# Optimization experiments

Measured on AMD Instinct MI355X. Metric: run time of the kernel, lower is better.

Reference implementation:

```python
import jax, jax.numpy as jnp
import numpy as np

N_NODES = 100000
N_EDGES = 6400000
NUM_FEATURES = 128
NUM_CLASSES = 10


def _gcn_norm(edge_index, num_nodes):
    # PyG GCNConv default: add self-loops, symmetric normalization
    src, dst = edge_index[0], edge_index[1]
    loop = jnp.arange(num_nodes, dtype=src.dtype)
    src = jnp.concatenate([src, loop])
    dst = jnp.concatenate([dst, loop])
    deg = jax.ops.segment_sum(jnp.ones_like(dst, dtype=jnp.float32), dst,
                              num_segments=num_nodes)
    dinv = jnp.where(deg > 0, jax.lax.rsqrt(deg), 0.0)
    norm = dinv[src] * dinv[dst]  # [E + N]
    return src, dst, norm


def _gcn_conv(x, W, b, src, dst, norm, num_nodes):
    h = x @ W                              # [N, out] small feature matmul
    msg = h[src] * norm[:, None]           # gather + per-edge scale
    agg = jax.ops.segment_sum(msg, dst, num_segments=num_nodes)  # scatter-add
    return agg + b


def setup_inputs() -> dict:
    key = jax.random.key(0)
    ks = jax.random.split(key, 10)
    x = jax.random.normal(ks[0], (N_NODES, NUM_FEATURES), dtype=jnp.float32)
    edge_index = jax.random.randint(ks[1], (2, N_EDGES), 0, N_NODES, dtype=jnp.int64)

    def glorot(k, shape):
        lim = np.sqrt(6.0 / (shape[0] + shape[1]))
        return jax.random.uniform(k, shape, jnp.float32, -lim, lim)

    return {
        "x": x,
        "edge_index": edge_index,
        "W1": glorot(ks[2], (NUM_FEATURES, 4)), "b1": jnp.zeros((4,), jnp.float32),
        "W2": glorot(ks[3], (4, 4)),            "b2": jnp.zeros((4,), jnp.float32),
        "W3": glorot(ks[4], (4, 2)),            "b3": jnp.zeros((2,), jnp.float32),
        "Wc": glorot(ks[5], (2, NUM_CLASSES)),  "bc": jnp.zeros((NUM_CLASSES,), jnp.float32),
    }


def reference(x, edge_index, W1, b1, W2, b2, W3, b3, Wc, bc):
    num_nodes = x.shape[0]
    src, dst, norm = _gcn_norm(edge_index, num_nodes)
    h = jnp.tanh(_gcn_conv(x, W1, b1, src, dst, norm, num_nodes))
    h = jnp.tanh(_gcn_conv(h, W2, b2, src, dst, norm, num_nodes))
    h = jnp.tanh(_gcn_conv(h, W3, b3, src, dst, norm, num_nodes))
    out = h @ Wc + bc
    return out, h
```

## Files before the change

### kernel.cpp

```cpp
#include <hip/hip_runtime.h>
#include <hip/hip_bf16.h>
#include <stdint.h>

#define N_NODES 100000
#define N_EDGES 6400000

#define NPB 128
#define NBKT 782
#define CAP 10752
#define SORT_CAP 9216
#define OUT_CAP (SORT_CAP + NPB * 3)
#define BIN_CHUNK 16384
#define BIN_THREADS 1024
#define SORT_THREADS 512
#define SORT_V4 5
#define NBIN_BLOCKS ((N_EDGES + BIN_CHUNK - 1) / BIN_CHUNK)


__global__ __launch_bounds__(1024) void k_bin(const void* __restrict__ ei,
                                              int* __restrict__ gcur,
                                              unsigned* __restrict__ perm1) {
  __shared__ unsigned staging[BIN_CHUNK];
  __shared__ int lcnt[1024];
  __shared__ int combo[1024];
  __shared__ int wsum[16];
  __shared__ int s_tot;
  __shared__ int s_th[3];
  __shared__ int s_is64;
  int t = threadIdx.x;
  lcnt[t] = 0;
  if (t < 64) {
    unsigned hv = ((const unsigned*)ei)[2 * t + 1];
    unsigned long long m = __ballot(hv != 0u);
    if (t == 0) s_is64 = (m == 0ull);
  }
  __syncthreads();
  int is64 = s_is64;
  size_t e0 = (size_t)blockIdx.x * BIN_CHUNK;
  int n = (int)(((e0 + BIN_CHUNK) <= N_EDGES) ? BIN_CHUNK : (N_EDGES - e0));

  if (is64) {
    const long long* e = (const long long*)ei;
    for (int k = 2 * t; k < n; k += 2048) {
      uint4 sp = *(const uint4*)(e + e0 + k);
      uint4 dp = *(const uint4*)(e + (size_t)N_EDGES + e0 + k);
      if (sp.x < N_NODES && dp.x < N_NODES) atomicAdd(&lcnt[dp.x >> 7], 1);
      if (sp.z < N_NODES && dp.z < N_NODES) atomicAdd(&lcnt[dp.z >> 7], 1);
    }
  } else {
    const unsigned* e = (const unsigned*)ei;
    for (int k = 4 * t; k < n; k += 4096) {
      uint4 sq = *(const uint4*)(e + e0 + k);
      uint4 dq = *(const uint4*)(e + (size_t)N_EDGES + e0 + k);
      if (sq.x < N_NODES && dq.x < N_NODES) atomicAdd(&lcnt[dq.x >> 7], 1);
      if (sq.y < N_NODES && dq.y < N_NODES) atomicAdd(&lcnt[dq.y >> 7], 1);
      if (sq.z < N_NODES && dq.z < N_NODES) atomicAdd(&lcnt[dq.z >> 7], 1);
      if (sq.w < N_NODES && dq.w < N_NODES) atomicAdd(&lcnt[dq.w >> 7], 1);
    }
  }
  __syncthreads();
  int c = lcnt[t];
  int lane = t & 63, w = t >> 6;
  int incl = c;
#pragma unroll
  for (int o = 1; o < 64; o <<= 1) {
    int u = __shfl_up(incl, o);
    if (lane >= o) incl += u;
  }
  if (lane == 63) wsum[w] = incl;
  __syncthreads();
  int wb = 0;
  for (int i = 0; i < w; ++i) wb += wsum[i];
  int excl = wb + incl - c;
  int gb = c ? atomicAdd(&gcur[t], c) : 0;
  lcnt[t] = excl;
  combo[t] = gb - excl;
  if (t == 256) s_th[0] = excl;
  if (t == 512) s_th[1] = excl;
  if (t == 768) s_th[2] = excl;
  if (t == 1023) s_tot = excl + c;
  __syncthreads();
  if (is64) {
    const long long* e = (const long long*)ei;
    for (int k = 2 * t; k < n; k += 2048) {
      uint4 sp = *(const uint4*)(e + e0 + k);
      uint4 dp = *(const uint4*)(e + (size_t)N_EDGES + e0 + k);
      if (sp.x < N_NODES && dp.x < N_NODES) {
        int p = atomicAdd(&lcnt[dp.x >> 7], 1);
        staging[p] = sp.x | ((dp.x & (NPB - 1u)) << 17) | (((dp.x >> 7) & 255u) << 24);
      }
      if (sp.z < N_NODES && dp.z < N_NODES) {
        int p = atomicAdd(&lcnt[dp.z >> 7], 1);
        staging[p] = sp.z | ((dp.z & (NPB - 1u)) << 17) | (((dp.z >> 7) & 255u) << 24);
      }
    }
  } else {
    const unsigned* e = (const unsigned*)ei;
    for (int k = 4 * t; k < n; k += 4096) {
      uint4 sq = *(const uint4*)(e + e0 + k);
      uint4 dq = *(const uint4*)(e + (size_t)N_EDGES + e0 + k);
      if (sq.x < N_NODES && dq.x < N_NODES) {
        int p = atomicAdd(&lcnt[dq.x >> 7], 1);
        staging[p] = sq.x | ((dq.x & (NPB - 1u)) << 17) | (((dq.x >> 7) & 255u) << 24);
      }
      if (sq.y < N_NODES && dq.y < N_NODES) {
        int p = atomicAdd(&lcnt[dq.y >> 7], 1);
        staging[p] = sq.y | ((dq.y & (NPB - 1u)) << 17) | (((dq.y >> 7) & 255u) << 24);
      }
      if (sq.z < N_NODES && dq.z < N_NODES) {
        int p = atomicAdd(&lcnt[dq.z >> 7], 1);
        staging[p] = sq.z | ((dq.z & (NPB - 1u)) << 17) | (((dq.z >> 7) & 255u) << 24);
      }
      if (sq.w < N_NODES && dq.w < N_NODES) {
        int p = atomicAdd(&lcnt[dq.w >> 7], 1);
        staging[p] = sq.w | ((dq.w & (NPB - 1u)) << 17) | (((dq.w >> 7) & 255u) << 24);
      }
    }
  }
  __syncthreads();
  int tot = s_tot, th0 = s_th[0], th1 = s_th[1], th2 = s_th[2];
  for (int j = t; j < tot; j += 1024) {
    unsigned r = staging[j];
    int hi = (j >= th0) + (j >= th1) + (j >= th2);
    int b = (int)(r >> 24) | (hi << 8);
    int o = combo[b] + j;
    if (o < CAP) perm1[(size_t)b * CAP + o] = r;
  }
}

__global__ __launch_bounds__(512) void k_sort(const int* __restrict__ gcur,
                                              const unsigned* __restrict__ perm1,
                                              unsigned* __restrict__ perm2,
                                              int2* __restrict__ offdeg,
                                              float* __restrict__ dinv) {
  __shared__ __align__(16) unsigned outbuf[OUT_CAP];
  __shared__ int h[NPB];
  __shared__ int wsum2[2];
  __shared__ int s_tot;
  int b = blockIdx.x, t = threadIdx.x;
  if (t < NPB) h[t] = 0;
  __syncthreads();
  int cnt = min(gcur[b], SORT_CAP);
  int base = b * CAP;
  unsigned rec[4 * SORT_V4];
  short rnk[4 * SORT_V4];
#pragma unroll
  for (int i = 0; i < SORT_V4; ++i) {
    int j = 4 * t + 2048 * i;
    uint4 q = *(const uint4*)(perm1 + base + j);
    rec[4 * i]     = (j     < cnt) ? q.x : 0xFFFFFFFFu;
    rec[4 * i + 1] = (j + 1 < cnt) ? q.y : 0xFFFFFFFFu;
    rec[4 * i + 2] = (j + 2 < cnt) ? q.z : 0xFFFFFFFFu;
    rec[4 * i + 3] = (j + 3 < cnt) ? q.w : 0xFFFFFFFFu;
  }
#pragma unroll
  for (int i = 0; i < 4 * SORT_V4; ++i) {
    rnk[i] = 0;
    if (rec[i] != 0xFFFFFFFFu)
      rnk[i] = (short)atomicAdd(&h[(rec[i] >> 17) & (NPB - 1)], 1);
  }
  __syncthreads();
  int degb = 0, degs4 = 0, incl = 0;
  if (t < NPB) {
    degb = h[t];
    degs4 = (degb + 3) & ~3;
    incl = degs4;
    int lane = t & 63;
#pragma unroll
    for (int o = 1; o < 64; o <<= 1) {
      int u = __shfl_up(incl, o);
      if (lane >= o) incl += u;
    }
    if (lane == 63) wsum2[t >> 6] = incl;
  }
  __syncthreads();
  int excl4 = 0;
  if (t < NPB) {
    excl4 = (t >= 64 ? wsum2[0] : 0) + incl - degs4;
    int node = b * NPB + t;
    if (node < N_NODES) {
      offdeg[node] = make_int2(base + excl4, degb);
      float dd = (float)degb + 1.0f;
      float y = rsqrtf(dd);
      y = y * (1.5f - 0.5f * dd * y * y);
      dinv[node] = y;
    }
    if (t == NPB - 1) s_tot = excl4 + degs4;
  }
  __syncthreads();
  if (t < NPB) h[t] = excl4;
  __syncthreads();
#pragma unroll
  for (int i = 0; i < 4 * SORT_V4; ++i) {
    if (rec[i] != 0xFFFFFFFFu)
      outbuf[h[(rec[i] >> 17) & (NPB - 1)] + rnk[i]] = rec[i] & 0x1FFFF;
  }
  __syncthreads();
  int tot = s_tot;
#pragma unroll
  for (int i = 0; i < SORT_V4; ++i) {
    int j = 4 * t + 2048 * i;
    if (j < tot)
      *(uint4*)(perm2 + base + j) = *(const uint4*)(outbuf + j);
  }
}

__global__ __launch_bounds__(256) void k_mm1(const float* __restrict__ x,
                                             const float* __restrict__ W1,
                                             const float* __restrict__ dinv,
                                             float* __restrict__ hs1) {
  int gid = blockIdx.x * blockDim.x + threadIdx.x;
  int node = gid >> 6;
  int lane = threadIdx.x & 63;
  if (node >= N_NODES) return;
  float2 v = ((const float2*)x)[(size_t)node * 64 + lane];
  float4 w0 = ((const float4*)W1)[2 * lane];
  float4 w1 = ((const float4*)W1)[2 * lane + 1];
  float a0 = v.x * w0.x + v.y * w1.x;
  float a1 = v.x * w0.y + v.y * w1.y;
  float a2 = v.x * w0.z + v.y * w1.z;
  float a3 = v.x * w0.w + v.y * w1.w;
#pragma unroll
  for (int off = 32; off > 0; off >>= 1) {
    a0 += __shfl_down(a0, off);
    a1 += __shfl_down(a1, off);
    a2 += __shfl_down(a2, off);
    a3 += __shfl_down(a3, off);
  }
  if (lane == 0) {
    float d = dinv[node];
    ((float4*)hs1)[node] = make_float4(d * a0, d * a1, d * a2, d * a3);
  }
}


__global__ __launch_bounds__(256) void k_l1(const int2* __restrict__ offdeg,
                                            const unsigned* __restrict__ perm2,
                                            const float* __restrict__ hs1,
                                            const float* __restrict__ dinv,
                                            const float* __restrict__ W2,
                                            const float* __restrict__ b1,
                                            float* __restrict__ hs2) {
  int node = blockIdx.x * 16 + (threadIdx.x >> 4);
  int l = threadIdx.x & 15;
  int2 od = offdeg[node];
  int base = od.x, d = od.y;
  float a0 = 0, a1 = 0, a2 = 0, a3 = 0;
  for (int j = 4 * l; j + 4 <= d; j += 64) {
    uint4 s = *(const uint4*)(perm2 + base + j);
    float4 v0 = ((const float4*)hs1)[s.x];
    float4 v1 = ((const float4*)hs1)[s.y];
    float4 v2 = ((const float4*)hs1)[s.z];
    float4 v3 = ((const float4*)hs1)[s.w];
    a0 += v0.x + v1.x + v2.x + v3.x;
    a1 += v0.y + v1.y + v2.y + v3.y;
    a2 += v0.z + v1.z + v2.z + v3.z;
    a3 += v0.w + v1.w + v2.w + v3.w;
  }
  int rb = d & ~3;
  if (l < d - rb) {
    float4 v = ((const float4*)hs1)[perm2[base + rb + l]];
    a0 += v.x; a1 += v.y; a2 += v.z; a3 += v.w;
  }
#pragma unroll
  for (int o = 8; o > 0; o >>= 1) {
    a0 += __shfl_down(a0, o); a1 += __shfl_down(a1, o);
    a2 += __shfl_down(a2, o); a3 += __shfl_down(a3, o);
  }
  if (l == 0) {
    float dn = dinv[node];
    float4 hl = ((const float4*)hs1)[node];
    float t0 = tanhf(dn * (a0 + hl.x) + b1[0]);
    float t1 = tanhf(dn * (a1 + hl.y) + b1[1]);
    float t2 = tanhf(dn * (a2 + hl.z) + b1[2]);
    float t3 = tanhf(dn * (a3 + hl.w) + b1[3]);
    float4 r;
    r.x = dn * (t0 * W2[0] + t1 * W2[4] + t2 * W2[8]  + t3 * W2[12]);
    r.y = dn * (t0 * W2[1] + t1 * W2[5] + t2 * W2[9]  + t3 * W2[13]);
    r.z = dn * (t0 * W2[2] + t1 * W2[6] + t2 * W2[10] + t3 * W2[14]);
    r.w = dn * (t0 * W2[3] + t1 * W2[7] + t2 * W2[11] + t3 * W2[15]);
    ((float4*)hs2)[node] = r;
  }
}

__global__ __launch_bounds__(256) void k_l2(const int2* __restrict__ offdeg,
                                            const unsigned* __restrict__ perm2,
                                            const float* __restrict__ hs2,
                                            const float* __restrict__ dinv,
                                            const float* __restrict__ W3,
                                            const float* __restrict__ b2,
                                            float* __restrict__ hs3) {
  int node = blockIdx.x * 16 + (threadIdx.x >> 4);
  int l = threadIdx.x & 15;
  int2 od = offdeg[node];
  int base = od.x, d = od.y;
  float a0 = 0, a1 = 0, a2 = 0, a3 = 0;
  for (int j = 4 * l; j + 4 <= d; j += 64) {
    uint4 s = *(const uint4*)(perm2 + base + j);
    float4 v0 = ((const float4*)hs2)[s.x];
    float4 v1 = ((const float4*)hs2)[s.y];
    float4 v2 = ((const float4*)hs2)[s.z];
    float4 v3 = ((const float4*)hs2)[s.w];
    a0 += v0.x + v1.x + v2.x + v3.x;
    a1 += v0.y + v1.y + v2.y + v3.y;
    a2 += v0.z + v1.z + v2.z + v3.z;
    a3 += v0.w + v1.w + v2.w + v3.w;
  }
  int rb = d & ~3;
  if (l < d - rb) {
    float4 v = ((const float4*)hs2)[perm2[base + rb + l]];
    a0 += v.x; a1 += v.y; a2 += v.z; a3 += v.w;
  }
#pragma unroll
  for (int o = 8; o > 0; o >>= 1) {
    a0 += __shfl_down(a0, o); a1 += __shfl_down(a1, o);
    a2 += __shfl_down(a2, o); a3 += __shfl_down(a3, o);
  }
  if (l == 0) {
    float dn = dinv[node];
    float4 hl = ((const float4*)hs2)[node];
    float t0 = tanhf(dn * (a0 + hl.x) + b2[0]);
    float t1 = tanhf(dn * (a1 + hl.y) + b2[1]);
    float t2 = tanhf(dn * (a2 + hl.z) + b2[2]);
    float t3 = tanhf(dn * (a3 + hl.w) + b2[3]);
    float2 r;
    r.x = dn * (t0 * W3[0] + t1 * W3[2] + t2 * W3[4] + t3 * W3[6]);
    r.y = dn * (t0 * W3[1] + t1 * W3[3] + t2 * W3[5] + t3 * W3[7]);
    ((float2*)hs3)[node] = r;
  }
}

__global__ __launch_bounds__(256) void k_l3(const int2* __restrict__ offdeg,
                                            const unsigned* __restrict__ perm2,
                                            const float* __restrict__ hs3,
                                            const float* __restrict__ dinv,
                                            const float* __restrict__ Wc,
                                            const float* __restrict__ bc,
                                            const float* __restrict__ b3,
                                            float* __restrict__ out) {
  int node = blockIdx.x * 16 + (threadIdx.x >> 4);
  int l = threadIdx.x & 15;
  int2 od = offdeg[node];
  int base = od.x, d = od.y;
  float a0 = 0, a1 = 0;
  for (int j = 4 * l; j + 4 <= d; j += 64) {
    uint4 s = *(const uint4*)(perm2 + base + j);
    float2 v0 = ((const float2*)hs3)[s.x];
    float2 v1 = ((const float2*)hs3)[s.y];
    float2 v2 = ((const float2*)hs3)[s.z];
    float2 v3 = ((const float2*)hs3)[s.w];
    a0 += v0.x + v1.x + v2.x + v3.x;
    a1 += v0.y + v1.y + v2.y + v3.y;
  }
  int rb = d & ~3;
  if (l < d - rb) {
    float2 v = ((const float2*)hs3)[perm2[base + rb + l]];
    a0 += v.x; a1 += v.y;
  }
#pragma unroll
  for (int o = 8; o > 0; o >>= 1) {
    a0 += __shfl_xor(a0, o); a1 += __shfl_xor(a1, o);
  }
  float dn = dinv[node];
  float2 hl = ((const float2*)hs3)[node];
  float t0 = tanhf(dn * (a0 + hl.x) + b3[0]);
  float t1 = tanhf(dn * (a1 + hl.y) + b3[1]);
  if (l < 10)
    out[(size_t)node * 10 + l] = t0 * Wc[l] + t1 * Wc[10 + l] + bc[l];
  else if (l == 10)
    out[(size_t)N_NODES * 10 + 2 * node + 0] = t0;
  else if (l == 11)
    out[(size_t)N_NODES * 10 + 2 * node + 1] = t1;
}

extern "C" void kernel_launch(void* const* d_in, const int* in_sizes, int n_in,
                              void* d_out, int out_size, void* d_ws, size_t ws_size,
                              hipStream_t stream) {
  const float* x  = (const float*)d_in[0];
  const void*  ei = d_in[1];
  const float* W1 = (const float*)d_in[2];
  const float* b1 = (const float*)d_in[3];
  const float* W2 = (const float*)d_in[4];
  const float* b2 = (const float*)d_in[5];
  const float* W3 = (const float*)d_in[6];
  const float* b3 = (const float*)d_in[7];
  const float* Wc = (const float*)d_in[8];
  const float* bc = (const float*)d_in[9];
  float* out = (float*)d_out;

  const size_t N = N_NODES;
  float* base = (float*)d_ws;
  float* dinv = base;
  float* hs1  = base + N;
  float* hs2  = base + 5 * N;
  float* hs3  = base + 9 * N;
  int2*  offdeg = (int2*)(base + 11 * N);
  int*   gcur = (int*)(base + 13 * N);
  unsigned* perm1 = (unsigned*)(base + 13 * N + 2048);
  unsigned* perm2 = perm1 + (size_t)NBKT * CAP;

  hipMemsetAsync(gcur, 0, 1024 * sizeof(int), stream);
  k_bin<<<NBIN_BLOCKS, BIN_THREADS, 0, stream>>>(ei, gcur, perm1);
  k_sort<<<NBKT, SORT_THREADS, 0, stream>>>(gcur, perm1, perm2, offdeg, dinv);
  k_mm1<<<(N_NODES * 64) / 256, 256, 0, stream>>>(x, W1, dinv, hs1);

  const int LB = N_NODES / 16;
  k_l1<<<LB, 256, 0, stream>>>(offdeg, perm2, hs1, dinv, W2, b1, hs2);
  k_l2<<<LB, 256, 0, stream>>>(offdeg, perm2, hs2, dinv, W3, b2, hs3);
  k_l3<<<LB, 256, 0, stream>>>(offdeg, perm2, hs3, dinv, Wc, bc, b3, out);
}
```

Before: 279.0 us.

## Drop src reads in bin counting and reload perm1 instead of register-held records in sort

The bin kernel's counting pass no longer loads source indices and filters only on destination range. The sort kernel moves to 1024 threads with fewer items per thread. Instead of keeping records and ranks in registers, it re-reads perm1 from global memory and uses shared atomics to place each record. This frees registers and saves bandwidth in counting, but placement within a node's bucket becomes nondeterministic and the counting filter may now disagree with the scatter pass if that pass still checks src.

Result: no change. 281.6 us (+1.0%).

```diff
diff --git a/kernel.cpp b/kernel.cpp
--- a/kernel.cpp
+++ b/kernel.cpp
@@ -12,8 +12,8 @@
 #define OUT_CAP (SORT_CAP + NPB * 3)
 #define BIN_CHUNK 16384
 #define BIN_THREADS 1024
-#define SORT_THREADS 512
-#define SORT_V4 5
+#define SORT_THREADS 1024
+#define SORT_V4 3
 #define NBIN_BLOCKS ((N_EDGES + BIN_CHUNK - 1) / BIN_CHUNK)
 
 
@@ -42,20 +42,18 @@
   if (is64) {
     const long long* e = (const long long*)ei;
     for (int k = 2 * t; k < n; k += 2048) {
-      uint4 sp = *(const uint4*)(e + e0 + k);
       uint4 dp = *(const uint4*)(e + (size_t)N_EDGES + e0 + k);
-      if (sp.x < N_NODES && dp.x < N_NODES) atomicAdd(&lcnt[dp.x >> 7], 1);
-      if (sp.z < N_NODES && dp.z < N_NODES) atomicAdd(&lcnt[dp.z >> 7], 1);
+      if (dp.x < N_NODES) atomicAdd(&lcnt[dp.x >> 7], 1);
+      if (dp.z < N_NODES) atomicAdd(&lcnt[dp.z >> 7], 1);
     }
   } else {
     const unsigned* e = (const unsigned*)ei;
     for (int k = 4 * t; k < n; k += 4096) {
-      uint4 sq = *(const uint4*)(e + e0 + k);
       uint4 dq = *(const uint4*)(e + (size_t)N_EDGES + e0 + k);
-      if (sq.x < N_NODES && dq.x < N_NODES) atomicAdd(&lcnt[dq.x >> 7], 1);
-      if (sq.y < N_NODES && dq.y < N_NODES) atomicAdd(&lcnt[dq.y >> 7], 1);
-      if (sq.z < N_NODES && dq.z < N_NODES) atomicAdd(&lcnt[dq.z >> 7], 1);
-      if (sq.w < N_NODES && dq.w < N_NODES) atomicAdd(&lcnt[dq.w >> 7], 1);
+      if (dq.x < N_NODES) atomicAdd(&lcnt[dq.x >> 7], 1);
+      if (dq.y < N_NODES) atomicAdd(&lcnt[dq.y >> 7], 1);
+      if (dq.z < N_NODES) atomicAdd(&lcnt[dq.z >> 7], 1);
+      if (dq.w < N_NODES) atomicAdd(&lcnt[dq.w >> 7], 1);
     }
   }
   __syncthreads();
@@ -128,11 +126,11 @@
   }
 }
 
-__global__ __launch_bounds__(512) void k_sort(const int* __restrict__ gcur,
-                                              const unsigned* __restrict__ perm1,
-                                              unsigned* __restrict__ perm2,
-                                              int2* __restrict__ offdeg,
-                                              float* __restrict__ dinv) {
+__global__ __launch_bounds__(1024) void k_sort(const int* __restrict__ gcur,
+                                               const unsigned* __restrict__ perm1,
+                                               unsigned* __restrict__ perm2,
+                                               int2* __restrict__ offdeg,
+                                               float* __restrict__ dinv) {
   __shared__ __align__(16) unsigned outbuf[OUT_CAP];
   __shared__ int h[NPB];
   __shared__ int wsum2[2];
@@ -142,22 +140,16 @@
   __syncthreads();
   int cnt = min(gcur[b], SORT_CAP);
   int base = b * CAP;
-  unsigned rec[4 * SORT_V4];
-  short rnk[4 * SORT_V4];
 #pragma unroll
   for (int i = 0; i < SORT_V4; ++i) {
-    int j = 4 * t + 2048 * i;
-    uint4 q = *(const uint4*)(perm1 + base + j);
-    rec[4 * i]     = (j     < cnt) ? q.x : 0xFFFFFFFFu;
-    rec[4 * i + 1] = (j + 1 < cnt) ? q.y : 0xFFFFFFFFu;
-    rec[4 * i + 2] = (j + 2 < cnt) ? q.z : 0xFFFFFFFFu;
-    rec[4 * i + 3] = (j + 3 < cnt) ? q.w : 0xFFFFFFFFu;
-  }
-#pragma unroll
-  for (int i = 0; i < 4 * SORT_V4; ++i) {
-    rnk[i] = 0;
-    if (rec[i] != 0xFFFFFFFFu)
-      rnk[i] = (short)atomicAdd(&h[(rec[i] >> 17) & (NPB - 1)], 1);
+    int j = 4 * t + 4096 * i;
+    if (j < cnt) {
+      uint4 q = *(const uint4*)(perm1 + base + j);
+      atomicAdd(&h[(q.x >> 17) & (NPB - 1)], 1);
+      if (j + 1 < cnt) atomicAdd(&h[(q.y >> 17) & (NPB - 1)], 1);
+      if (j + 2 < cnt) atomicAdd(&h[(q.z >> 17) & (NPB - 1)], 1);
+      if (j + 3 < cnt) atomicAdd(&h[(q.w >> 17) & (NPB - 1)], 1);
+    }
   }
   __syncthreads();
   int degb = 0, degs4 = 0, incl = 0;
@@ -191,15 +183,21 @@
   if (t < NPB) h[t] = excl4;
   __syncthreads();
 #pragma unroll
-  for (int i = 0; i < 4 * SORT_V4; ++i) {
-    if (rec[i] != 0xFFFFFFFFu)
-      outbuf[h[(rec[i] >> 17) & (NPB - 1)] + rnk[i]] = rec[i] & 0x1FFFF;
+  for (int i = 0; i < SORT_V4; ++i) {
+    int j = 4 * t + 4096 * i;
+    if (j < cnt) {
+      uint4 q = *(const uint4*)(perm1 + base + j);
+      { int p = atomicAdd(&h[(q.x >> 17) & (NPB - 1)], 1); outbuf[p] = q.x & 0x1FFFF; }
+      if (j + 1 < cnt) { int p = atomicAdd(&h[(q.y >> 17) & (NPB - 1)], 1); outbuf[p] = q.y & 0x1FFFF; }
+      if (j + 2 < cnt) { int p = atomicAdd(&h[(q.z >> 17) & (NPB - 1)], 1); outbuf[p] = q.z & 0x1FFFF; }
+      if (j + 3 < cnt) { int p = atomicAdd(&h[(q.w >> 17) & (NPB - 1)], 1); outbuf[p] = q.w & 0x1FFFF; }
+    }
   }
   __syncthreads();
   int tot = s_tot;
 #pragma unroll
   for (int i = 0; i < SORT_V4; ++i) {
-    int j = 4 * t + 2048 * i;
+    int j = 4 * t + 4096 * i;
     if (j < tot)
       *(uint4*)(perm2 + base + j) = *(const uint4*)(outbuf + j);
   }
```
